# Kernel tuning notes

Measured on AMD Instinct MI355X. Metric: run time of the kernel, lower is better.

The kernel has to match this reference:

```python
import jax, jax.numpy as jnp
import numpy as np

B, D, C, P = 64, 262144, 4, 4096  # batch, original_dim, c, proj_dim


def setup_inputs() -> dict:
    key = jax.random.key(0)
    kx, ki, ks = jax.random.split(key, 3)
    x = jax.random.normal(kx, (B, D), dtype=jnp.float32)
    rand_indices = jax.random.randint(ki, (D, C), 0, P, dtype=jnp.int64)
    rand_sign_bits = jax.random.randint(ks, (D, C), 0, 2, dtype=jnp.int32)
    return {"x": x, "rand_indices": rand_indices, "rand_sign_bits": rand_sign_bits}


def reference(x, rand_indices, rand_sign_bits):
    # signs in {-1, +1}, matching (randint(0,2)*2 - 1) in the torch module
    signs = (2 * rand_sign_bits - 1).astype(x.dtype)          # [D, C]
    idx = rand_indices.reshape(-1)                             # [D*C]
    vals = (x[:, :, None] * signs[None, :, :]).reshape(x.shape[0], -1)  # [B, D*C]
    # scatter-add each signed value into its hashed projection slot
    project = lambda v: jax.ops.segment_sum(v, idx, num_segments=P)
    return jax.vmap(project)(vals)                             # [B, P]
```

## Files before the change

kernel.cpp:

```cpp
#include <hip/hip_runtime.h>
#include <hip/hip_bf16.h>
#include <hip/hip_fp16.h>


constexpr int B_DIM = 64;
constexpr int D_DIM = 262144;
constexpr int P_DIM = 4096;

constexpr int NDS   = 64;
constexpr int SLICE = D_DIM / NDS;
constexpr int NBIN  = 16;
constexpr int NSC   = 16;
constexpr int SC_D  = SLICE / NSC;
constexpr int BCAP  = 128;
constexpr int WPB   = 8;
constexpr int PR_W  = 32;
constexpr int NPR   = P_DIM / PR_W;
constexpr int QCAP_E = 28;

constexpr size_t REG_OFF   = 0;
constexpr size_t REG_BYTES = (size_t)NDS * NSC * NBIN * BCAP * 4;
constexpr size_t CNT_OFF   = REG_OFF + REG_BYTES;
constexpr size_t CNT_BYTES = (size_t)NDS * NSC * NBIN * 4;
constexpr size_t XT_OFF    = CNT_OFF + CNT_BYTES;
constexpr size_t XT_BYTES  = (size_t)D_DIM * B_DIM * 2;
constexpr size_t PART_OFF  = XT_OFF + XT_BYTES;
constexpr size_t PART_BYTES = (size_t)NPR * NDS * PR_W * B_DIM * 2;
constexpr size_t WS_NEED   = PART_OFF + PART_BYTES;

__global__ __launch_bounds__(512) void k_binpack(
    const int* __restrict__ idx, const int* __restrict__ sgn,
    unsigned* __restrict__ reg, int* __restrict__ cnt) {
    const int w = threadIdx.x >> 6, lane = threadIdx.x & 63;
    const int dslice = blockIdx.x >> 1;
    const int half   = blockIdx.x & 1;
    const int sc     = half * 8 + w;
    const int d0     = dslice * SLICE + sc * SC_D;
    unsigned* regw = reg + ((size_t)(dslice * NSC + sc) * NBIN) * BCAP;
    const unsigned long long lmask = (1ull << lane) - 1ull;

    unsigned cb[16];
    #pragma unroll
    for (int b = 0; b < 16; ++b) cb[b] = 0;

    #pragma unroll
    for (int step = 0; step < SC_D / 64; ++step) {
        const int dli = step * 64 + lane;
        const int4 iv = reinterpret_cast<const int4*>(idx)[d0 + dli];
        const int4 sv = reinterpret_cast<const int4*>(sgn)[d0 + dli];
        const unsigned rowbyte = (unsigned)((sc * SC_D + dli) << 7);
        #pragma unroll
        for (int c = 0; c < 4; ++c) {
            const unsigned p = ((unsigned)((c==0)?iv.x:(c==1)?iv.y:(c==2)?iv.z:iv.w)) & 4095u;
            const unsigned s = ((unsigned)((c==0)?sv.x:(c==1)?sv.y:(c==2)?sv.z:sv.w)) & 1u;
            const unsigned e = rowbyte | ((p & 255u) << 19) | ((s ^ 1u) << 31);
            const unsigned bin = p >> 8;
            unsigned pos = 0;
            #pragma unroll
            for (int b = 0; b < 16; ++b) {
                const unsigned long long m = __ballot(bin == (unsigned)b);
                if (bin == (unsigned)b) pos = cb[b] + (unsigned)__popcll(m & lmask);
                cb[b] += (unsigned)__popcll(m);
            }
            if (pos < (unsigned)BCAP) regw[bin * BCAP + pos] = e;
        }
    }
    unsigned cval = 0;
    #pragma unroll
    for (int b = 0; b < 16; ++b) {
        const unsigned cc = cb[b] < (unsigned)BCAP ? cb[b] : (unsigned)BCAP;
        cval = (lane == b) ? cc : cval;
    }
    if (lane < 16) cnt[(dslice * NSC + sc) * NBIN + lane] = (int)cval;
}

__device__ __forceinline__ unsigned short f32_to_bf16_rne(float f) {
    unsigned u = __float_as_uint(f);
    u += 0x7FFFu + ((u >> 16) & 1u);
    return (unsigned short)(u >> 16);
}

__global__ __launch_bounds__(256) void k_transpose(
    const float* __restrict__ x, unsigned short* __restrict__ xTb) {
    __shared__ float tile[64 * 65];
    const int d0 = blockIdx.x * 64;
    const int t = threadIdx.x;
    const int lane = t & 63;
    #pragma unroll
    for (int k = 0; k < 16; ++k) {
        const int b = k * 4 + (t >> 6);
        tile[lane * 65 + b] = x[(size_t)b * D_DIM + d0 + lane];
    }
    __syncthreads();
    #pragma unroll
    for (int k = 0; k < 16; ++k) {
        const int dr = k * 4 + (t >> 6);
        xTb[(size_t)(d0 + dr) * B_DIM + lane] = f32_to_bf16_rne(tile[dr * 65 + lane]);
    }
}

__global__ __launch_bounds__(512, 8) void k_process(
    const unsigned* __restrict__ reg, const int* __restrict__ cnt,
    const unsigned short* __restrict__ xTb, __half* __restrict__ part) {
    __shared__ __half2 hist[WPB][PR_W * 32];
    __shared__ unsigned short q[WPB][NSC][QCAP_E];
    __shared__ short qcnt[WPB][NSC];

    const int w = threadIdx.x >> 6, lane = threadIdx.x & 63;
    const int dslice = blockIdx.x & 63;
    const int bin    = blockIdx.x >> 6;

    __half2* h2 = hist[w];
    {
        unsigned* h32 = reinterpret_cast<unsigned*>(h2);
        #pragma unroll
        for (int k = 0; k < 16; ++k) h32[k * 64 + lane] = 0u;
    }

    const unsigned long long lmask = (1ull << lane) - 1ull;

    #pragma unroll
    for (int h = 0; h < 2; ++h) {
        const int sc = 2 * w + h;
        const int n  = cnt[(dslice * NSC + sc) * NBIN + bin];
        const unsigned* list = reg + ((size_t)((dslice * NSC + sc) * NBIN + bin)) * BCAP;
        unsigned qc[8];
        #pragma unroll
        for (int b = 0; b < 8; ++b) qc[b] = 0;
        for (int base = 0; base < n; base += 64) {
            const int i = base + lane;
            const bool valid = i < n;
            const unsigned e = valid ? list[i] : 0u;
            const unsigned t = valid ? ((e >> 24) & 7u) : 8u;
            const unsigned e16 = ((e >> 7) & 255u) | (((e >> 19) & 31u) << 8)
                               | ((e >> 31) << 15);
            unsigned pos = 0;
            #pragma unroll
            for (int b = 0; b < 8; ++b) {
                const unsigned long long m = __ballot(t == (unsigned)b);
                if (t == (unsigned)b) pos = qc[b] + (unsigned)__popcll(m & lmask);
                qc[b] += (unsigned)__popcll(m);
            }
            if (valid && pos < (unsigned)QCAP_E)
                q[t][sc][pos] = (unsigned short)e16;
        }
        unsigned cval = 0;
        #pragma unroll
        for (int b = 0; b < 8; ++b) {
            const unsigned cc = qc[b] < (unsigned)QCAP_E ? qc[b] : (unsigned)QCAP_E;
            cval = (lane == b) ? cc : cval;
        }
        if (lane < 8) qcnt[lane][sc] = (short)cval;
    }
    __syncthreads();

    const char* xs_c = reinterpret_cast<const char*>(xTb) + (size_t)dslice * SLICE * 128;
    const unsigned li4 = (unsigned)(lane & 31) * 4u;
    const bool hi = lane >= 32;

    auto pair_rmw = [&](unsigned wrd, unsigned dv) {
        const unsigned poL = (wrd >> 8) & 31u, poH = (wrd >> 24) & 31u;
        const unsigned smL = (wrd & 0x8000u)     ? 0x80008000u : 0u;
        const unsigned smH = (wrd & 0x80000000u) ? 0x80008000u : 0u;
        const float flo = __uint_as_float(dv << 16);
        const float fhh = __uint_as_float(dv & 0xFFFF0000u);
        unsigned pkb = __builtin_bit_cast(unsigned, __floats2half2_rn(flo, fhh));
        pkb ^= hi ? smH : smL;
        const unsigned a = (hi ? poH : poL) * 32u + (unsigned)(lane & 31);
        if (poL != poH) {
            const __half2 v2 = __builtin_bit_cast(__half2, pkb);
            h2[a] = __hadd2(h2[a], v2);
        } else {
            const unsigned other = (unsigned)__shfl((int)pkb, (lane & 31) + 32);
            if (!hi) {
                const __half2 vsum = __hadd2(__builtin_bit_cast(__half2, pkb),
                                             __builtin_bit_cast(__half2, other));
                h2[a] = __hadd2(h2[a], vsum);
            }
        }
    };

    for (int s = 0; s < NSC; ++s) {
        const int n = qcnt[w][s];
        const unsigned* qs32 = reinterpret_cast<const unsigned*>(&q[w][s][0]);
        const unsigned sb = (unsigned)s << 15;
        int i = 0;
        for (; i + 4 <= n; i += 4) {
            const unsigned wa = __builtin_amdgcn_readfirstlane(qs32[i >> 1]);
            const unsigned wb = __builtin_amdgcn_readfirstlane(qs32[(i >> 1) + 1]);
            const unsigned vaA = sb + ((hi ? (wa >> 16) : wa) & 255u) * 128u + li4;
            const unsigned vaB = sb + ((hi ? (wb >> 16) : wb) & 255u) * 128u + li4;
            const unsigned dA = *reinterpret_cast<const unsigned*>(xs_c + vaA);
            const unsigned dB = *reinterpret_cast<const unsigned*>(xs_c + vaB);
            pair_rmw(wa, dA);
            pair_rmw(wb, dB);
        }
        for (; i + 2 <= n; i += 2) {
            const unsigned wa = __builtin_amdgcn_readfirstlane(qs32[i >> 1]);
            const unsigned va = sb + ((hi ? (wa >> 16) : wa) & 255u) * 128u + li4;
            pair_rmw(wa, *reinterpret_cast<const unsigned*>(xs_c + va));
        }
        if (i < n) {
            const unsigned e0 = __builtin_amdgcn_readfirstlane((unsigned)q[w][s][i]);
            if (!hi) {
                const unsigned va = sb + (e0 & 255u) * 128u + li4;
                const unsigned dv = *reinterpret_cast<const unsigned*>(xs_c + va);
                const float flo = __uint_as_float(dv << 16);
                const float fhh = __uint_as_float(dv & 0xFFFF0000u);
                unsigned pkb = __builtin_bit_cast(unsigned, __floats2half2_rn(flo, fhh));
                pkb ^= (e0 & 0x8000u) ? 0x80008000u : 0u;
                const __half2 v2 = __builtin_bit_cast(__half2, pkb);
                const unsigned a = ((e0 >> 8) & 31u) * 32u + (unsigned)(lane & 31);
                h2[a] = __hadd2(h2[a], v2);
            }
        }
    }

    unsigned* wp32 = reinterpret_cast<unsigned*>(
        part + ((size_t)((bin * WPB + w) * NDS + dslice)) * (PR_W * B_DIM));
    const unsigned* h32 = reinterpret_cast<const unsigned*>(h2);
    #pragma unroll
    for (int k = 0; k < 16; ++k)
        wp32[k * 64 + lane] = h32[k * 64 + lane];
}

__global__ __launch_bounds__(256) void k_reduce(
    const __half* __restrict__ part, float* __restrict__ out) {
    const int pr = blockIdx.x;
    const int pq = blockIdx.y;
    const int t  = threadIdx.x;

    float4 acc = make_float4(0.f, 0.f, 0.f, 0.f);
    const size_t base = (size_t)pr * NDS * (PR_W * B_DIM) + (size_t)pq * 1024;
    for (int ds = 0; ds < NDS; ++ds) {
        const uint2 pv = *reinterpret_cast<const uint2*>(
            part + base + (size_t)ds * (PR_W * B_DIM) + t * 4);
        const __half2 h0 = __builtin_bit_cast(__half2, pv.x);
        const __half2 h1 = __builtin_bit_cast(__half2, pv.y);
        acc.x += __half2float(h0.x); acc.y += __half2float(h0.y);
        acc.z += __half2float(h1.x); acc.w += __half2float(h1.y);
    }

    __shared__ float st[16][65];
    const int po = (t * 4) >> 6;
    const int b0 = (t * 4) & 63;
    st[po][b0]     = acc.x; st[po][b0 + 1] = acc.y;
    st[po][b0 + 2] = acc.z; st[po][b0 + 3] = acc.w;
    __syncthreads();

    #pragma unroll
    for (int k = 0; k < 4; ++k) {
        const int flat = k * 256 + t;
        const int b = flat >> 4, poo = flat & 15;
        out[(size_t)b * P_DIM + pr * PR_W + pq * 16 + poo] = st[poo][b];
    }
}

__device__ __forceinline__ float signed_val(float x, int s) {
    return __uint_as_float(__float_as_uint(x) ^ (((unsigned)(s ^ 1)) << 31));
}

__global__ __launch_bounds__(1024) void sjlt_hist_fb(
    const float* __restrict__ x, const int* __restrict__ idx,
    const int* __restrict__ sgn, float* __restrict__ out) {
    __shared__ float hist[2][P_DIM];
    for (int i = threadIdx.x; i < 2 * P_DIM; i += 1024) (&hist[0][0])[i] = 0.0f;
    __syncthreads();
    const int chunk = blockIdx.x, bg = blockIdx.y;
    const int d0 = chunk * (D_DIM / 16), b0 = bg * 2;
    const float* xr0 = x + (size_t)b0 * D_DIM + d0;
    const float* xr1 = xr0 + D_DIM;
    const int4* iv4 = reinterpret_cast<const int4*>(idx) + d0;
    const int4* sv4 = reinterpret_cast<const int4*>(sgn) + d0;
    for (int t = threadIdx.x; t < D_DIM / 16; t += 1024) {
        const int4 iv = iv4[t]; const int4 sv = sv4[t];
        const float x0 = xr0[t], x1 = xr1[t];
        unsafeAtomicAdd(&hist[0][iv.x], signed_val(x0, sv.x));
        unsafeAtomicAdd(&hist[0][iv.y], signed_val(x0, sv.y));
        unsafeAtomicAdd(&hist[0][iv.z], signed_val(x0, sv.z));
        unsafeAtomicAdd(&hist[0][iv.w], signed_val(x0, sv.w));
        unsafeAtomicAdd(&hist[1][iv.x], signed_val(x1, sv.x));
        unsafeAtomicAdd(&hist[1][iv.y], signed_val(x1, sv.y));
        unsafeAtomicAdd(&hist[1][iv.z], signed_val(x1, sv.z));
        unsafeAtomicAdd(&hist[1][iv.w], signed_val(x1, sv.w));
    }
    __syncthreads();
    float* o = out + (size_t)b0 * P_DIM;
    for (int p = threadIdx.x; p < P_DIM; p += 1024) {
        unsafeAtomicAdd(&o[p],         hist[0][p]);
        unsafeAtomicAdd(&o[P_DIM + p], hist[1][p]);
    }
}

extern "C" void kernel_launch(void* const* d_in, const int* in_sizes, int n_in,
                              void* d_out, int out_size, void* d_ws, size_t ws_size,
                              hipStream_t stream) {
    const float* x   = (const float*)d_in[0];
    const int*   idx = (const int*)d_in[1];
    const int*   sgn = (const int*)d_in[2];
    float* out = (float*)d_out;

    if (ws_size >= WS_NEED) {
        char* ws = (char*)d_ws;
        unsigned* reg = (unsigned*)(ws + REG_OFF);
        int* cnt      = (int*)(ws + CNT_OFF);
        unsigned short* xTb = (unsigned short*)(ws + XT_OFF);
        __half* part  = (__half*)(ws + PART_OFF);

        k_binpack<<<NDS * 2, 512, 0, stream>>>(idx, sgn, reg, cnt);
        k_transpose<<<D_DIM / 64, 256, 0, stream>>>(x, xTb);
        k_process<<<NBIN * NDS, 512, 0, stream>>>(reg, cnt, xTb, part);
        k_reduce<<<dim3(NPR, 2), 256, 0, stream>>>(part, out);
    } else {
        hipMemsetAsync(d_out, 0, (size_t)out_size * sizeof(float), stream);
        dim3 grid(16, 32);
        sjlt_hist_fb<<<grid, 1024, 0, stream>>>(x, idx, sgn, out);
    }
}
```

Before: 76.57 us.

## Split process bins in half and use block-wide compaction into per-warp entry lists

The process kernel now covers half a projection bin per block, doubling the grid. Entries from all sub-chunks are compacted block-wide into one per-warp list via ballot counts and prefix bases. The inner loop handles eight entries at a time, merging colliding slots in registers before the read-modify-write. Low and high half-waves accumulate into separate histograms that are summed at writeback. This trades extra ballot and compaction work and more blocks for fewer LDS conflicts and better latency hiding, and it relies on the entry word layout produced by binpack.

Result: no change. 77.11 us (+0.7%).

```diff
diff --git a/kernel.cpp b/kernel.cpp
--- a/kernel.cpp
+++ b/kernel.cpp
@@ -13,10 +13,11 @@
 constexpr int NSC   = 16;
 constexpr int SC_D  = SLICE / NSC;
 constexpr int BCAP  = 128;
+constexpr int NHB   = 32;
 constexpr int WPB   = 8;
-constexpr int PR_W  = 32;
+constexpr int PR_W  = 16;
 constexpr int NPR   = P_DIM / PR_W;
-constexpr int QCAP_E = 28;
+constexpr int LCAP  = 128;
 
 constexpr size_t REG_OFF   = 0;
 constexpr size_t REG_BYTES = (size_t)NDS * NSC * NBIN * BCAP * 4;
@@ -102,136 +103,233 @@
 __global__ __launch_bounds__(512, 8) void k_process(
     const unsigned* __restrict__ reg, const int* __restrict__ cnt,
     const unsigned short* __restrict__ xTb, __half* __restrict__ part) {
-    __shared__ __half2 hist[WPB][PR_W * 32];
-    __shared__ unsigned short q[WPB][NSC][QCAP_E];
-    __shared__ short qcnt[WPB][NSC];
+    __shared__ __half2 hist[WPB][2 * PR_W * 32];
+    __shared__ unsigned lst[WPB][LCAP];
+    __shared__ int cnts[WPB][WPB];
+    __shared__ int baseL[WPB][WPB];
+    __shared__ int totals[WPB];
 
     const int w = threadIdx.x >> 6, lane = threadIdx.x & 63;
     const int dslice = blockIdx.x & 63;
-    const int bin    = blockIdx.x >> 6;
-
-    __half2* h2 = hist[w];
+    const int hb  = blockIdx.x >> 6;
+    const int bin = hb >> 1, half = hb & 1;
+
+    __half2* hw = hist[w];
     {
-        unsigned* h32 = reinterpret_cast<unsigned*>(h2);
+        unsigned* h32 = reinterpret_cast<unsigned*>(hw);
         #pragma unroll
         for (int k = 0; k < 16; ++k) h32[k * 64 + lane] = 0u;
     }
 
     const unsigned long long lmask = (1ull << lane) - 1ull;
 
-    #pragma unroll
-    for (int h = 0; h < 2; ++h) {
-        const int sc = 2 * w + h;
+    unsigned er[4];
+    int n0 = 0, n1 = 0;
+    int c0 = 0, c1 = 0, c2 = 0, c3 = 0, c4 = 0, c5 = 0, c6 = 0, c7 = 0;
+    #pragma unroll
+    for (int sc2 = 0; sc2 < 2; ++sc2) {
+        const int sc = 2 * w + sc2;
         const int n  = cnt[(dslice * NSC + sc) * NBIN + bin];
         const unsigned* list = reg + ((size_t)((dslice * NSC + sc) * NBIN + bin)) * BCAP;
-        unsigned qc[8];
-        #pragma unroll
-        for (int b = 0; b < 8; ++b) qc[b] = 0;
-        for (int base = 0; base < n; base += 64) {
-            const int i = base + lane;
-            const bool valid = i < n;
-            const unsigned e = valid ? list[i] : 0u;
-            const unsigned t = valid ? ((e >> 24) & 7u) : 8u;
-            const unsigned e16 = ((e >> 7) & 255u) | (((e >> 19) & 31u) << 8)
-                               | ((e >> 31) << 15);
-            unsigned pos = 0;
-            #pragma unroll
-            for (int b = 0; b < 8; ++b) {
-                const unsigned long long m = __ballot(t == (unsigned)b);
-                if (t == (unsigned)b) pos = qc[b] + (unsigned)__popcll(m & lmask);
-                qc[b] += (unsigned)__popcll(m);
+        if (sc2 == 0) n0 = n; else n1 = n;
+        #pragma unroll
+        for (int b = 0; b < 2; ++b) {
+            const int i = b * 64 + lane;
+            const unsigned e = (i < n) ? list[i] : 0u;
+            er[sc2 * 2 + b] = e;
+            const unsigned po8 = (e >> 19) & 255u;
+            const bool valid = (i < n) && ((int)(po8 >> 7) == half);
+            const unsigned t = valid ? ((po8 >> 4) & 7u) : 0xFFu;
+            const unsigned long long m0 = __ballot(t == 0u);
+            const unsigned long long m1 = __ballot(t == 1u);
+            const unsigned long long m2 = __ballot(t == 2u);
+            const unsigned long long m3 = __ballot(t == 3u);
+            const unsigned long long m4 = __ballot(t == 4u);
+            const unsigned long long m5 = __ballot(t == 5u);
+            const unsigned long long m6 = __ballot(t == 6u);
+            const unsigned long long m7 = __ballot(t == 7u);
+            c0 += __popcll(m0); c1 += __popcll(m1);
+            c2 += __popcll(m2); c3 += __popcll(m3);
+            c4 += __popcll(m4); c5 += __popcll(m5);
+            c6 += __popcll(m6); c7 += __popcll(m7);
+        }
+    }
+    {
+        int cval = 0;
+        cval = (lane == 0) ? c0 : cval; cval = (lane == 1) ? c1 : cval;
+        cval = (lane == 2) ? c2 : cval; cval = (lane == 3) ? c3 : cval;
+        cval = (lane == 4) ? c4 : cval; cval = (lane == 5) ? c5 : cval;
+        cval = (lane == 6) ? c6 : cval; cval = (lane == 7) ? c7 : cval;
+        if (lane < 8) cnts[w][lane] = cval;
+    }
+    __syncthreads();
+
+    if (w == 0 && lane < 8) {
+        int run = 0;
+        #pragma unroll
+        for (int ww = 0; ww < 8; ++ww) { baseL[lane][ww] = run; run += cnts[ww][lane]; }
+        totals[lane] = run;
+    }
+    __syncthreads();
+
+    c0 = c1 = c2 = c3 = c4 = c5 = c6 = c7 = 0;
+    #pragma unroll
+    for (int sc2 = 0; sc2 < 2; ++sc2) {
+        const int n = (sc2 == 0) ? n0 : n1;
+        #pragma unroll
+        for (int b = 0; b < 2; ++b) {
+            const int i = b * 64 + lane;
+            const unsigned e = er[sc2 * 2 + b];
+            const unsigned po8 = (e >> 19) & 255u;
+            const bool valid = (i < n) && ((int)(po8 >> 7) == half);
+            const unsigned t = valid ? ((po8 >> 4) & 7u) : 0xFFu;
+            const unsigned long long m0 = __ballot(t == 0u);
+            const unsigned long long m1 = __ballot(t == 1u);
+            const unsigned long long m2 = __ballot(t == 2u);
+            const unsigned long long m3 = __ballot(t == 3u);
+            const unsigned long long m4 = __ballot(t == 4u);
+            const unsigned long long m5 = __ballot(t == 5u);
+            const unsigned long long m6 = __ballot(t == 6u);
+            const unsigned long long m7 = __ballot(t == 7u);
+            if (valid) {
+                const unsigned long long mt =
+                    t < 4u ? (t < 2u ? (t == 0u ? m0 : m1) : (t == 2u ? m2 : m3))
+                           : (t < 6u ? (t == 4u ? m4 : m5) : (t == 6u ? m6 : m7));
+                const int cbase =
+                    t < 4u ? (t < 2u ? (t == 0u ? c0 : c1) : (t == 2u ? c2 : c3))
+                           : (t < 6u ? (t == 4u ? c4 : c5) : (t == 6u ? c6 : c7));
+                const int pos = baseL[t][w] + cbase + (int)__popcll(mt & lmask);
+                if (pos < LCAP) lst[t][pos] = e;
             }
-            if (valid && pos < (unsigned)QCAP_E)
-                q[t][sc][pos] = (unsigned short)e16;
-        }
-        unsigned cval = 0;
-        #pragma unroll
-        for (int b = 0; b < 8; ++b) {
-            const unsigned cc = qc[b] < (unsigned)QCAP_E ? qc[b] : (unsigned)QCAP_E;
-            cval = (lane == b) ? cc : cval;
-        }
-        if (lane < 8) qcnt[lane][sc] = (short)cval;
+            c0 += __popcll(m0); c1 += __popcll(m1);
+            c2 += __popcll(m2); c3 += __popcll(m3);
+            c4 += __popcll(m4); c5 += __popcll(m5);
+            c6 += __popcll(m6); c7 += __popcll(m7);
+        }
     }
     __syncthreads();
 
     const char* xs_c = reinterpret_cast<const char*>(xTb) + (size_t)dslice * SLICE * 128;
     const unsigned li4 = (unsigned)(lane & 31) * 4u;
     const bool hi = lane >= 32;
-
-    auto pair_rmw = [&](unsigned wrd, unsigned dv) {
-        const unsigned poL = (wrd >> 8) & 31u, poH = (wrd >> 24) & 31u;
-        const unsigned smL = (wrd & 0x8000u)     ? 0x80008000u : 0u;
-        const unsigned smH = (wrd & 0x80000000u) ? 0x80008000u : 0u;
+    const unsigned l31 = (unsigned)(lane & 31);
+    const int n = totals[w] < LCAP ? totals[w] : LCAP;
+    const unsigned* L = lst[w];
+
+    int i = 0;
+    for (; i + 8 <= n; i += 8) {
+        const uint4 A  = *reinterpret_cast<const uint4*>(L + i);
+        const uint4 Bv = *reinterpret_cast<const uint4*>(L + i + 4);
+        const unsigned e0 = __builtin_amdgcn_readfirstlane(A.x);
+        const unsigned e1 = __builtin_amdgcn_readfirstlane(A.y);
+        const unsigned e2 = __builtin_amdgcn_readfirstlane(A.z);
+        const unsigned e3 = __builtin_amdgcn_readfirstlane(A.w);
+        const unsigned e4 = __builtin_amdgcn_readfirstlane(Bv.x);
+        const unsigned e5 = __builtin_amdgcn_readfirstlane(Bv.y);
+        const unsigned e6 = __builtin_amdgcn_readfirstlane(Bv.z);
+        const unsigned e7 = __builtin_amdgcn_readfirstlane(Bv.w);
+        const unsigned va0 = (hi ? (e4 & 0x7FFFFu) : (e0 & 0x7FFFFu)) + li4;
+        const unsigned va1 = (hi ? (e5 & 0x7FFFFu) : (e1 & 0x7FFFFu)) + li4;
+        const unsigned va2 = (hi ? (e6 & 0x7FFFFu) : (e2 & 0x7FFFFu)) + li4;
+        const unsigned va3 = (hi ? (e7 & 0x7FFFFu) : (e3 & 0x7FFFFu)) + li4;
+        const unsigned d0 = *reinterpret_cast<const unsigned*>(xs_c + va0);
+        const unsigned d1 = *reinterpret_cast<const unsigned*>(xs_c + va1);
+        const unsigned d2 = *reinterpret_cast<const unsigned*>(xs_c + va2);
+        const unsigned d3 = *reinterpret_cast<const unsigned*>(xs_c + va3);
+
+        const unsigned pL0 = (e0 >> 19) & 15u, pL1 = (e1 >> 19) & 15u;
+        const unsigned pL2 = (e2 >> 19) & 15u, pL3 = (e3 >> 19) & 15u;
+        const unsigned pH0 = (e4 >> 19) & 15u, pH1 = (e5 >> 19) & 15u;
+        const unsigned pH2 = (e6 >> 19) & 15u, pH3 = (e7 >> 19) & 15u;
+
+        __half2 v[4];
+        #pragma unroll
+        for (int k = 0; k < 4; ++k) {
+            const unsigned dv = (k == 0) ? d0 : (k == 1) ? d1 : (k == 2) ? d2 : d3;
+            const unsigned eL = (k == 0) ? e0 : (k == 1) ? e1 : (k == 2) ? e2 : e3;
+            const unsigned eH = (k == 0) ? e4 : (k == 1) ? e5 : (k == 2) ? e6 : e7;
+            const float flo = __uint_as_float(dv << 16);
+            const float fhh = __uint_as_float(dv & 0xFFFF0000u);
+            unsigned pkb = __builtin_bit_cast(unsigned, __floats2half2_rn(flo, fhh));
+            const unsigned sm = hi ? (eH & 0x80000000u) : (eL & 0x80000000u);
+            pkb ^= sm ? 0x80008000u : 0u;
+            v[k] = __builtin_bit_cast(__half2, pkb);
+        }
+
+        const __half2 zero2 = __builtin_bit_cast(__half2, 0u);
+        {
+            const bool m01 = hi ? (pH0 == pH1) : (pL0 == pL1);
+            v[1] = m01 ? __hadd2(v[1], v[0]) : v[1];  v[0] = m01 ? zero2 : v[0];
+            const bool m02 = hi ? (pH0 == pH2) : (pL0 == pL2);
+            v[2] = m02 ? __hadd2(v[2], v[0]) : v[2];  v[0] = m02 ? zero2 : v[0];
+            const bool m12 = hi ? (pH1 == pH2) : (pL1 == pL2);
+            v[2] = m12 ? __hadd2(v[2], v[1]) : v[2];  v[1] = m12 ? zero2 : v[1];
+            const bool m03 = hi ? (pH0 == pH3) : (pL0 == pL3);
+            v[3] = m03 ? __hadd2(v[3], v[0]) : v[3];  v[0] = m03 ? zero2 : v[0];
+            const bool m13 = hi ? (pH1 == pH3) : (pL1 == pL3);
+            v[3] = m13 ? __hadd2(v[3], v[1]) : v[3];  v[1] = m13 ? zero2 : v[1];
+            const bool m23 = hi ? (pH2 == pH3) : (pL2 == pL3);
+            v[3] = m23 ? __hadd2(v[3], v[2]) : v[3];  v[2] = m23 ? zero2 : v[2];
+        }
+
+        const unsigned a0 = (hi ? (512u + pH0 * 32u) : (pL0 * 32u)) + l31;
+        const unsigned a1 = (hi ? (512u + pH1 * 32u) : (pL1 * 32u)) + l31;
+        const unsigned a2 = (hi ? (512u + pH2 * 32u) : (pL2 * 32u)) + l31;
+        const unsigned a3 = (hi ? (512u + pH3 * 32u) : (pL3 * 32u)) + l31;
+        const __half2 h0 = hw[a0];
+        const __half2 h1 = hw[a1];
+        const __half2 h2v = hw[a2];
+        const __half2 h3 = hw[a3];
+        hw[a0] = __hadd2(h0, v[0]);
+        hw[a1] = __hadd2(h1, v[1]);
+        hw[a2] = __hadd2(h2v, v[2]);
+        hw[a3] = __hadd2(h3, v[3]);
+    }
+    for (; i + 2 <= n; i += 2) {
+        const unsigned eA = __builtin_amdgcn_readfirstlane(L[i]);
+        const unsigned eB = __builtin_amdgcn_readfirstlane(L[i + 1]);
+        const unsigned va = (hi ? (eB & 0x7FFFFu) : (eA & 0x7FFFFu)) + li4;
+        const unsigned dv = *reinterpret_cast<const unsigned*>(xs_c + va);
         const float flo = __uint_as_float(dv << 16);
         const float fhh = __uint_as_float(dv & 0xFFFF0000u);
         unsigned pkb = __builtin_bit_cast(unsigned, __floats2half2_rn(flo, fhh));
-        pkb ^= hi ? smH : smL;
-        const unsigned a = (hi ? poH : poL) * 32u + (unsigned)(lane & 31);
-        if (poL != poH) {
-            const __half2 v2 = __builtin_bit_cast(__half2, pkb);
-            h2[a] = __hadd2(h2[a], v2);
-        } else {
-            const unsigned other = (unsigned)__shfl((int)pkb, (lane & 31) + 32);
-            if (!hi) {
-                const __half2 vsum = __hadd2(__builtin_bit_cast(__half2, pkb),
-                                             __builtin_bit_cast(__half2, other));
-                h2[a] = __hadd2(h2[a], vsum);
-            }
-        }
-    };
-
-    for (int s = 0; s < NSC; ++s) {
-        const int n = qcnt[w][s];
-        const unsigned* qs32 = reinterpret_cast<const unsigned*>(&q[w][s][0]);
-        const unsigned sb = (unsigned)s << 15;
-        int i = 0;
-        for (; i + 4 <= n; i += 4) {
-            const unsigned wa = __builtin_amdgcn_readfirstlane(qs32[i >> 1]);
-            const unsigned wb = __builtin_amdgcn_readfirstlane(qs32[(i >> 1) + 1]);
-            const unsigned vaA = sb + ((hi ? (wa >> 16) : wa) & 255u) * 128u + li4;
-            const unsigned vaB = sb + ((hi ? (wb >> 16) : wb) & 255u) * 128u + li4;
-            const unsigned dA = *reinterpret_cast<const unsigned*>(xs_c + vaA);
-            const unsigned dB = *reinterpret_cast<const unsigned*>(xs_c + vaB);
-            pair_rmw(wa, dA);
-            pair_rmw(wb, dB);
-        }
-        for (; i + 2 <= n; i += 2) {
-            const unsigned wa = __builtin_amdgcn_readfirstlane(qs32[i >> 1]);
-            const unsigned va = sb + ((hi ? (wa >> 16) : wa) & 255u) * 128u + li4;
-            pair_rmw(wa, *reinterpret_cast<const unsigned*>(xs_c + va));
-        }
-        if (i < n) {
-            const unsigned e0 = __builtin_amdgcn_readfirstlane((unsigned)q[w][s][i]);
-            if (!hi) {
-                const unsigned va = sb + (e0 & 255u) * 128u + li4;
-                const unsigned dv = *reinterpret_cast<const unsigned*>(xs_c + va);
-                const float flo = __uint_as_float(dv << 16);
-                const float fhh = __uint_as_float(dv & 0xFFFF0000u);
-                unsigned pkb = __builtin_bit_cast(unsigned, __floats2half2_rn(flo, fhh));
-                pkb ^= (e0 & 0x8000u) ? 0x80008000u : 0u;
-                const __half2 v2 = __builtin_bit_cast(__half2, pkb);
-                const unsigned a = ((e0 >> 8) & 31u) * 32u + (unsigned)(lane & 31);
-                h2[a] = __hadd2(h2[a], v2);
-            }
+        const unsigned sm = hi ? (eB & 0x80000000u) : (eA & 0x80000000u);
+        pkb ^= sm ? 0x80008000u : 0u;
+        const unsigned po = hi ? ((eB >> 19) & 15u) : ((eA >> 19) & 15u);
+        const unsigned a = (hi ? (512u + po * 32u) : (po * 32u)) + l31;
+        hw[a] = __hadd2(hw[a], __builtin_bit_cast(__half2, pkb));
+    }
+    if (i < n) {
+        const unsigned eA = __builtin_amdgcn_readfirstlane(L[i]);
+        if (!hi) {
+            const unsigned va = (eA & 0x7FFFFu) + li4;
+            const unsigned dv = *reinterpret_cast<const unsigned*>(xs_c + va);
+            const float flo = __uint_as_float(dv << 16);
+            const float fhh = __uint_as_float(dv & 0xFFFF0000u);
+            unsigned pkb = __builtin_bit_cast(unsigned, __floats2half2_rn(flo, fhh));
+            pkb ^= (eA & 0x80000000u) ? 0x80008000u : 0u;
+            const unsigned a = ((eA >> 19) & 15u) * 32u + l31;
+            hw[a] = __hadd2(hw[a], __builtin_bit_cast(__half2, pkb));
         }
     }
 
     unsigned* wp32 = reinterpret_cast<unsigned*>(
-        part + ((size_t)((bin * WPB + w) * NDS + dslice)) * (PR_W * B_DIM));
-    const unsigned* h32 = reinterpret_cast<const unsigned*>(h2);
-    #pragma unroll
-    for (int k = 0; k < 16; ++k)
-        wp32[k * 64 + lane] = h32[k * 64 + lane];
+        part + ((size_t)((hb * WPB + w) * NDS + dslice)) * (PR_W * B_DIM));
+    #pragma unroll
+    for (int k = 0; k < 8; ++k) {
+        const int idxw = k * 64 + lane;
+        const __half2 s = __hadd2(hw[idxw], hw[512 + idxw]);
+        wp32[idxw] = __builtin_bit_cast(unsigned, s);
+    }
 }
 
 __global__ __launch_bounds__(256) void k_reduce(
     const __half* __restrict__ part, float* __restrict__ out) {
     const int pr = blockIdx.x;
-    const int pq = blockIdx.y;
     const int t  = threadIdx.x;
 
     float4 acc = make_float4(0.f, 0.f, 0.f, 0.f);
-    const size_t base = (size_t)pr * NDS * (PR_W * B_DIM) + (size_t)pq * 1024;
+    const size_t base = (size_t)pr * NDS * (PR_W * B_DIM);
     for (int ds = 0; ds < NDS; ++ds) {
         const uint2 pv = *reinterpret_cast<const uint2*>(
             part + base + (size_t)ds * (PR_W * B_DIM) + t * 4);
@@ -252,7 +350,7 @@
     for (int k = 0; k < 4; ++k) {
         const int flat = k * 256 + t;
         const int b = flat >> 4, poo = flat & 15;
-        out[(size_t)b * P_DIM + pr * PR_W + pq * 16 + poo] = st[poo][b];
+        out[(size_t)b * P_DIM + pr * PR_W + poo] = st[poo][b];
     }
 }
 
@@ -309,8 +407,8 @@
 
         k_binpack<<<NDS * 2, 512, 0, stream>>>(idx, sgn, reg, cnt);
         k_transpose<<<D_DIM / 64, 256, 0, stream>>>(x, xTb);
-        k_process<<<NBIN * NDS, 512, 0, stream>>>(reg, cnt, xTb, part);
-        k_reduce<<<dim3(NPR, 2), 256, 0, stream>>>(part, out);
+        k_process<<<NHB * NDS, 512, 0, stream>>>(reg, cnt, xTb, part);
+        k_reduce<<<NPR, 256, 0, stream>>>(part, out);
     } else {
         hipMemsetAsync(d_out, 0, (size_t)out_size * sizeof(float), stream);
         dim3 grid(16, 32);
```

## Fuse transpose and binpack into one prep kernel, store x as fp16

Applied to the files above, without the earlier changes.

Merges the x-transpose kernel and the index bin-packing kernel into a single launch, with blocks split by blockIdx between the two jobs. The binpack part now runs in 256-thread blocks covering quarters of each slice. The transposed copy of x is stored directly as fp16 instead of bf16, so the process kernel no longer converts bf16 to half2 on every gathered element. This saves one launch and lets the two independent prep jobs overlap, and it trims ALU work in the hot loop. In exchange it drops the bf16 range safety for fp16 rounding of x values.

Result: faster. 72.34 us (median of 2 runs) (-5.5%).

```diff
diff --git a/kernel.cpp b/kernel.cpp
--- a/kernel.cpp
+++ b/kernel.cpp
@@ -18,6 +18,9 @@
 constexpr int NPR   = P_DIM / PR_W;
 constexpr int QCAP_E = 28;
 
+constexpr int TRANS_BLOCKS = D_DIM / 64;
+constexpr int BINPK_BLOCKS = NDS * 4;
+
 constexpr size_t REG_OFF   = 0;
 constexpr size_t REG_BYTES = (size_t)NDS * NSC * NBIN * BCAP * 4;
 constexpr size_t CNT_OFF   = REG_OFF + REG_BYTES;
@@ -28,14 +31,38 @@
 constexpr size_t PART_BYTES = (size_t)NPR * NDS * PR_W * B_DIM * 2;
 constexpr size_t WS_NEED   = PART_OFF + PART_BYTES;
 
-__global__ __launch_bounds__(512) void k_binpack(
+__global__ __launch_bounds__(256) void k_prep(
+    const float* __restrict__ x,
     const int* __restrict__ idx, const int* __restrict__ sgn,
+    unsigned short* __restrict__ xTh,
     unsigned* __restrict__ reg, int* __restrict__ cnt) {
-    const int w = threadIdx.x >> 6, lane = threadIdx.x & 63;
-    const int dslice = blockIdx.x >> 1;
-    const int half   = blockIdx.x & 1;
-    const int sc     = half * 8 + w;
-    const int d0     = dslice * SLICE + sc * SC_D;
+    __shared__ float tile[64 * 65];
+    const int t = threadIdx.x;
+    const int lane = t & 63;
+
+    if (blockIdx.x < TRANS_BLOCKS) {
+        const int d0 = blockIdx.x * 64;
+        #pragma unroll
+        for (int k = 0; k < 16; ++k) {
+            const int b = k * 4 + (t >> 6);
+            tile[lane * 65 + b] = x[(size_t)b * D_DIM + d0 + lane];
+        }
+        __syncthreads();
+        #pragma unroll
+        for (int k = 0; k < 16; ++k) {
+            const int dr = k * 4 + (t >> 6);
+            const __half h = __float2half_rn(tile[dr * 65 + lane]);
+            xTh[(size_t)(d0 + dr) * B_DIM + lane] = __builtin_bit_cast(unsigned short, h);
+        }
+        return;
+    }
+
+    const int bid = blockIdx.x - TRANS_BLOCKS;
+    const int w = t >> 6;
+    const int dslice  = bid >> 2;
+    const int quarter = bid & 3;
+    const int sc      = quarter * 4 + w;
+    const int d0      = dslice * SLICE + sc * SC_D;
     unsigned* regw = reg + ((size_t)(dslice * NSC + sc) * NBIN) * BCAP;
     const unsigned long long lmask = (1ull << lane) - 1ull;
 
@@ -74,34 +101,9 @@
     if (lane < 16) cnt[(dslice * NSC + sc) * NBIN + lane] = (int)cval;
 }
 
-__device__ __forceinline__ unsigned short f32_to_bf16_rne(float f) {
-    unsigned u = __float_as_uint(f);
-    u += 0x7FFFu + ((u >> 16) & 1u);
-    return (unsigned short)(u >> 16);
-}
-
-__global__ __launch_bounds__(256) void k_transpose(
-    const float* __restrict__ x, unsigned short* __restrict__ xTb) {
-    __shared__ float tile[64 * 65];
-    const int d0 = blockIdx.x * 64;
-    const int t = threadIdx.x;
-    const int lane = t & 63;
-    #pragma unroll
-    for (int k = 0; k < 16; ++k) {
-        const int b = k * 4 + (t >> 6);
-        tile[lane * 65 + b] = x[(size_t)b * D_DIM + d0 + lane];
-    }
-    __syncthreads();
-    #pragma unroll
-    for (int k = 0; k < 16; ++k) {
-        const int dr = k * 4 + (t >> 6);
-        xTb[(size_t)(d0 + dr) * B_DIM + lane] = f32_to_bf16_rne(tile[dr * 65 + lane]);
-    }
-}
-
 __global__ __launch_bounds__(512, 8) void k_process(
     const unsigned* __restrict__ reg, const int* __restrict__ cnt,
-    const unsigned short* __restrict__ xTb, __half* __restrict__ part) {
+    const unsigned short* __restrict__ xTh, __half* __restrict__ part) {
     __shared__ __half2 hist[WPB][PR_W * 32];
     __shared__ unsigned short q[WPB][NSC][QCAP_E];
     __shared__ short qcnt[WPB][NSC];
@@ -154,7 +156,7 @@
     }
     __syncthreads();
 
-    const char* xs_c = reinterpret_cast<const char*>(xTb) + (size_t)dslice * SLICE * 128;
+    const char* xs_c = reinterpret_cast<const char*>(xTh) + (size_t)dslice * SLICE * 128;
     const unsigned li4 = (unsigned)(lane & 31) * 4u;
     const bool hi = lane >= 32;
 
@@ -162,10 +164,7 @@
         const unsigned poL = (wrd >> 8) & 31u, poH = (wrd >> 24) & 31u;
         const unsigned smL = (wrd & 0x8000u)     ? 0x80008000u : 0u;
         const unsigned smH = (wrd & 0x80000000u) ? 0x80008000u : 0u;
-        const float flo = __uint_as_float(dv << 16);
-        const float fhh = __uint_as_float(dv & 0xFFFF0000u);
-        unsigned pkb = __builtin_bit_cast(unsigned, __floats2half2_rn(flo, fhh));
-        pkb ^= hi ? smH : smL;
+        const unsigned pkb = dv ^ (hi ? smH : smL);
         const unsigned a = (hi ? poH : poL) * 32u + (unsigned)(lane & 31);
         if (poL != poH) {
             const __half2 v2 = __builtin_bit_cast(__half2, pkb);
@@ -205,10 +204,7 @@
             if (!hi) {
                 const unsigned va = sb + (e0 & 255u) * 128u + li4;
                 const unsigned dv = *reinterpret_cast<const unsigned*>(xs_c + va);
-                const float flo = __uint_as_float(dv << 16);
-                const float fhh = __uint_as_float(dv & 0xFFFF0000u);
-                unsigned pkb = __builtin_bit_cast(unsigned, __floats2half2_rn(flo, fhh));
-                pkb ^= (e0 & 0x8000u) ? 0x80008000u : 0u;
+                const unsigned pkb = dv ^ ((e0 & 0x8000u) ? 0x80008000u : 0u);
                 const __half2 v2 = __builtin_bit_cast(__half2, pkb);
                 const unsigned a = ((e0 >> 8) & 31u) * 32u + (unsigned)(lane & 31);
                 h2[a] = __hadd2(h2[a], v2);
@@ -304,12 +300,11 @@
         char* ws = (char*)d_ws;
         unsigned* reg = (unsigned*)(ws + REG_OFF);
         int* cnt      = (int*)(ws + CNT_OFF);
-        unsigned short* xTb = (unsigned short*)(ws + XT_OFF);
+        unsigned short* xTh = (unsigned short*)(ws + XT_OFF);
         __half* part  = (__half*)(ws + PART_OFF);
 
-        k_binpack<<<NDS * 2, 512, 0, stream>>>(idx, sgn, reg, cnt);
-        k_transpose<<<D_DIM / 64, 256, 0, stream>>>(x, xTb);
-        k_process<<<NBIN * NDS, 512, 0, stream>>>(reg, cnt, xTb, part);
+        k_prep<<<TRANS_BLOCKS + BINPK_BLOCKS, 256, 0, stream>>>(x, idx, sgn, xTh, reg, cnt);
+        k_process<<<NBIN * NDS, 512, 0, stream>>>(reg, cnt, xTh, part);
         k_reduce<<<dim3(NPR, 2), 256, 0, stream>>>(part, out);
     } else {
         hipMemsetAsync(d_out, 0, (size_t)out_size * sizeof(float), stream);
```
